# Performance work log

Hardware: AMD Instinct MI355X
Metric: run time of the kernel (lower is better)

## Reference

```python
import jax, jax.numpy as jnp
import numpy as np

N = 8192        # total mesh nodes
M1 = 6000       # nodes set from x (full 3D coords)
M2 = 2000       # nodes set from y (coords 0 and 2 only)
B = 4           # batch
K = 4           # smoothing steps


def setup_inputs() -> dict:
    key = jax.random.key(0)
    k1, k2, k3, k4 = jax.random.split(key, 4)
    # Sparse-ish random symmetric-flavored adjacency, stored dense (as the module does).
    A = (jax.random.uniform(k1, (N, N)) < 0.002).astype(jnp.float32)
    idx = jnp.arange(N)
    # Ring edges guarantee every row has degree >= 1 (avoid divide-by-zero).
    A = A.at[idx, (idx + 1) % N].set(1.0)
    A = A.at[(idx + 1) % N, idx].set(1.0)
    # Diagonal: 1 for first half, 0 for second half -> output mask selects N//2 nodes.
    A = A.at[idx, idx].set((idx < N // 2).astype(jnp.float32))
    # Disjoint index sets for the scatter writes.
    perm = jax.random.permutation(k2, N)
    li1 = perm[:M1].astype(jnp.int64)
    li2 = perm[M1:M1 + M2].astype(jnp.int64)
    x = jax.random.normal(k3, (B, M1 * 3), dtype=jnp.float32)
    y = jax.random.normal(k4, (B, M2 * 2), dtype=jnp.float32)
    temp_zero = jnp.zeros((N, 3), dtype=jnp.float32)
    return {"x": x, "y": y, "edge_matrix": A, "temp_zero": temp_zero,
            "local_indices_1": li1, "local_indices_2": li2, "k": K}


def reference(x, y, edge_matrix, temp_zero, local_indices_1, local_indices_2, k):
    b = x.shape[0]
    # Scatter-build the graph state [B, N, 3].
    temp = jnp.broadcast_to(temp_zero[None], (b,) + temp_zero.shape)
    temp = temp.at[:, local_indices_1, :].set(x.reshape(b, -1, 3))
    y2 = y.reshape(b, -1, 2)
    temp = temp.at[:, local_indices_2, 0].set(y2[:, :, 0])
    temp = temp.at[:, local_indices_2, 2].set(y2[:, :, 1])
    # Degree normalization vector (row sums), computed once.
    deg = jnp.sum(edge_matrix, axis=1)  # [N]
    mesh = temp
    for _ in range(k):
        # smoother: (mesh^T @ A^T)^T == A @ mesh over the node dim, then /degree.
        mesh = jnp.einsum('ij,bjc->bic', edge_matrix, mesh) / deg[None, :, None]
    # Gather rows whose diagonal adjacency entry is zero.
    mask = jnp.diag(edge_matrix) == 0
    return mesh[:, mask, :]
```

## Files before the change

kernel.cpp:

```cpp
#include <hip/hip_runtime.h>

#define NN   8192
#define NNP  (NN + 4)
#define NN3  (NN * 3)
#define NNP3 (NNP * 3)
#define CAP  64
#define M1   6000
#define M2   2000
#define SENT NN

typedef unsigned short u16;

__global__ __launch_bounds__(256) void build_ell(const float* __restrict__ A,
                                                 u16* __restrict__ cols,
                                                 int* __restrict__ nch,
                                                 float* __restrict__ rdeg,
                                                 float* __restrict__ mesh_a,
                                                 float* __restrict__ mesh_b,
                                                 int B) {
    __shared__ int cnt;
    const int row = blockIdx.x;
    const int tid = threadIdx.x;

    {
        const int tot = B * NNP3;
        const int g = blockIdx.x * 256 + tid;
        if (g < tot) mesh_a[g] = 0.f;
        if (blockIdx.x == 0 && tid < B * 12) {
            const int b = tid / 12, r = tid - b * 12;
            mesh_b[b * NNP3 + NN * 3 + r] = 0.f;
        }
    }

    if (tid == 0) cnt = 0;
    __syncthreads();
    const float4* __restrict__ Arow = (const float4*)(A + (size_t)row * NN);
    float4 v[8];
    #pragma unroll
    for (int k = 0; k < 8; ++k) v[k] = Arow[k * 256 + tid];
    u16* __restrict__ crow = cols + row * CAP;
    #pragma unroll
    for (int k = 0; k < 8; ++k) {
        const int base = (k * 256 + tid) * 4;
        if (v[k].x != 0.f) { int p = atomicAdd(&cnt, 1); if (p < CAP) crow[p] = (u16)(base);     }
        if (v[k].y != 0.f) { int p = atomicAdd(&cnt, 1); if (p < CAP) crow[p] = (u16)(base + 1); }
        if (v[k].z != 0.f) { int p = atomicAdd(&cnt, 1); if (p < CAP) crow[p] = (u16)(base + 2); }
        if (v[k].w != 0.f) { int p = atomicAdd(&cnt, 1); if (p < CAP) crow[p] = (u16)(base + 3); }
    }
    __syncthreads();
    int c = cnt;
    if (c > CAP) c = CAP;
    const int padded = (c + 7) & ~7;
    if (tid < padded - c && c + tid < CAP) crow[c + tid] = (u16)SENT;
    if (tid == 0) {
        nch[row]  = padded >> 3;
        rdeg[row] = 1.0f / (float)cnt;
    }
}

__global__ __launch_bounds__(256) void scatter_xy(const float* __restrict__ x,
                                                  const float* __restrict__ y,
                                                  const int* __restrict__ li1,
                                                  const int* __restrict__ li2,
                                                  float* __restrict__ mesh_a, int B) {
    const int g = blockIdx.x * 256 + threadIdx.x;
    const int nx = B * M1 * 3, ny = B * M2 * 2;
    if (g < nx) {
        const int b = g / (M1 * 3);
        const int rem = g - b * (M1 * 3);
        const int j = rem / 3, c = rem - j * 3;
        mesh_a[b * NNP3 + li1[j] * 3 + c] = x[g];
    } else if (g < nx + ny) {
        const int h = g - nx;
        const int b = h / (M2 * 2);
        const int rem = h - b * (M2 * 2);
        const int j = rem / 2, c2 = rem & 1;
        mesh_a[b * NNP3 + li2[j] * 3 + (c2 ? 2 : 0)] = y[h];
    }
}

__global__ __launch_bounds__(256) void spmv_full(const u16* __restrict__ cols,
                                                 const int* __restrict__ nch,
                                                 const float* __restrict__ rdeg,
                                                 const float* __restrict__ src,
                                                 float* __restrict__ dst, int B) {
    const int g = blockIdx.x * 256 + threadIdx.x;
    if (g >= B * NN3) return;
    const int b = g / NN3;
    const int r = g - b * NN3;
    const int i = r / 3, c = r - i * 3;
    const float* __restrict__ mb = src + b * NNP3;
    const uint4* __restrict__ cr = (const uint4*)(cols + i * CAP);
    const int n = nch[i];
    float acc = 0.f;
    for (int ch = 0; ch < n; ++ch) {
        const uint4 q = cr[ch];
        acc += mb[(q.x & 0xFFFF) * 3 + c] + mb[(q.x >> 16) * 3 + c]
             + mb[(q.y & 0xFFFF) * 3 + c] + mb[(q.y >> 16) * 3 + c]
             + mb[(q.z & 0xFFFF) * 3 + c] + mb[(q.z >> 16) * 3 + c]
             + mb[(q.w & 0xFFFF) * 3 + c] + mb[(q.w >> 16) * 3 + c];
    }
    dst[b * NNP3 + i * 3 + c] = acc * rdeg[i];
}

__global__ __launch_bounds__(256) void spmv_last(const u16* __restrict__ cols,
                                                 const int* __restrict__ nch,
                                                 const float* __restrict__ rdeg,
                                                 const float* __restrict__ src,
                                                 float* __restrict__ out, int B) {
    const int H3 = (NN / 2) * 3;
    const int g = blockIdx.x * 256 + threadIdx.x;
    if (g >= B * H3) return;
    const int b = g / H3;
    const int r = g - b * H3;
    const int i2 = r / 3, c = r - i2 * 3;
    const int i = NN / 2 + i2;
    const float* __restrict__ mb = src + b * NNP3;
    const uint4* __restrict__ cr = (const uint4*)(cols + i * CAP);
    const int n = nch[i];
    float acc = 0.f;
    for (int ch = 0; ch < n; ++ch) {
        const uint4 q = cr[ch];
        acc += mb[(q.x & 0xFFFF) * 3 + c] + mb[(q.x >> 16) * 3 + c]
             + mb[(q.y & 0xFFFF) * 3 + c] + mb[(q.y >> 16) * 3 + c]
             + mb[(q.z & 0xFFFF) * 3 + c] + mb[(q.z >> 16) * 3 + c]
             + mb[(q.w & 0xFFFF) * 3 + c] + mb[(q.w >> 16) * 3 + c];
    }
    out[g] = acc * rdeg[i];
}

extern "C" void kernel_launch(void* const* d_in, const int* in_sizes, int n_in,
                              void* d_out, int out_size, void* d_ws, size_t ws_size,
                              hipStream_t stream) {
    const float* x   = (const float*)d_in[0];
    const float* y   = (const float*)d_in[1];
    const float* A   = (const float*)d_in[2];
    const int*   li1 = (const int*)d_in[4];
    const int*   li2 = (const int*)d_in[5];

    const int B = in_sizes[0] / (M1 * 3);

    char* ws = (char*)d_ws;
    u16*   cols   = (u16*)ws;    ws += (size_t)NN * CAP * 2;
    int*   nchv   = (int*)ws;    ws += (size_t)NN * 4;
    float* rdeg   = (float*)ws;  ws += (size_t)NN * 4;
    float* mesh_a = (float*)ws;  ws += (size_t)B * NNP3 * 4;
    float* mesh_b = (float*)ws;

    build_ell<<<NN, 256, 0, stream>>>(A, cols, nchv, rdeg, mesh_a, mesh_b, B);

    const int sc_total = B * M1 * 3 + B * M2 * 2;
    scatter_xy<<<(sc_total + 255) / 256, 256, 0, stream>>>(x, y, li1, li2, mesh_a, B);

    const int full = B * NN3;
    const int nbf = (full + 255) / 256;
    spmv_full<<<nbf, 256, 0, stream>>>(cols, nchv, rdeg, mesh_a, mesh_b, B);
    spmv_full<<<nbf, 256, 0, stream>>>(cols, nchv, rdeg, mesh_b, mesh_a, B);
    spmv_full<<<nbf, 256, 0, stream>>>(cols, nchv, rdeg, mesh_a, mesh_b, B);

    const int half = B * (NN / 2) * 3;
    spmv_last<<<(half + 255) / 256, 256, 0, stream>>>(cols, nchv, rdeg, mesh_b,
                                                      (float*)d_out, B);
}
```

Before: 70.83 us.

## Fuse scatter and four SpMV passes into one cooperative kernel with grid sync

Replaces the dense zero-fill of mesh_a and the scatter kernel with a per-node encoding table (enc) that the first SpMV pass reads to fetch x/y values directly. The four SpMV launches are merged into a single cooperative kernel with grid.sync between steps, which removes launch gaps and the full-buffer memset. In exchange, the first pass adds an extra indirection per neighbour, and the cooperative launch requires all 384 blocks to be co-resident; grid.sync has its own cost.

New measurement: 216.6 us. 206% more time.

```diff
diff --git a/kernel.cpp b/kernel.cpp
--- a/kernel.cpp
+++ b/kernel.cpp
@@ -1,4 +1,7 @@
 #include <hip/hip_runtime.h>
+#include <hip/hip_cooperative_groups.h>
+
+namespace cg = cooperative_groups;
 
 #define NN   8192
 #define NNP  (NN + 4)
@@ -8,6 +11,8 @@
 #define M1   6000
 #define M2   2000
 #define SENT NN
+#define CB   384
+#define CT   256
 
 typedef unsigned short u16;
 
@@ -15,23 +20,29 @@
                                                  u16* __restrict__ cols,
                                                  int* __restrict__ nch,
                                                  float* __restrict__ rdeg,
+                                                 int* __restrict__ enc,
                                                  float* __restrict__ mesh_a,
                                                  float* __restrict__ mesh_b,
+                                                 const int* __restrict__ li1,
+                                                 const int* __restrict__ li2,
                                                  int B) {
-    __shared__ int cnt;
     const int row = blockIdx.x;
     const int tid = threadIdx.x;
 
-    {
-        const int tot = B * NNP3;
-        const int g = blockIdx.x * 256 + tid;
-        if (g < tot) mesh_a[g] = 0.f;
-        if (blockIdx.x == 0 && tid < B * 12) {
+    if (row == NN) {
+        for (int i = tid; i < NNP; i += 256) enc[i] = 0;
+        if (tid < B * 12) {
             const int b = tid / 12, r = tid - b * 12;
+            mesh_a[b * NNP3 + NN * 3 + r] = 0.f;
             mesh_b[b * NNP3 + NN * 3 + r] = 0.f;
         }
+        __syncthreads();
+        for (int j = tid; j < M1; j += 256) enc[li1[j]] = (j << 2) | 1;
+        for (int j = tid; j < M2; j += 256) enc[li2[j]] = (j << 2) | 2;
+        return;
     }
 
+    __shared__ int cnt;
     if (tid == 0) cnt = 0;
     __syncthreads();
     const float4* __restrict__ Arow = (const float4*)(A + (size_t)row * NN);
@@ -58,75 +69,78 @@
     }
 }
 
-__global__ __launch_bounds__(256) void scatter_xy(const float* __restrict__ x,
-                                                  const float* __restrict__ y,
-                                                  const int* __restrict__ li1,
-                                                  const int* __restrict__ li2,
-                                                  float* __restrict__ mesh_a, int B) {
-    const int g = blockIdx.x * 256 + threadIdx.x;
-    const int nx = B * M1 * 3, ny = B * M2 * 2;
-    if (g < nx) {
-        const int b = g / (M1 * 3);
-        const int rem = g - b * (M1 * 3);
-        const int j = rem / 3, c = rem - j * 3;
-        mesh_a[b * NNP3 + li1[j] * 3 + c] = x[g];
-    } else if (g < nx + ny) {
-        const int h = g - nx;
-        const int b = h / (M2 * 2);
-        const int rem = h - b * (M2 * 2);
-        const int j = rem / 2, c2 = rem & 1;
-        mesh_a[b * NNP3 + li2[j] * 3 + (c2 ? 2 : 0)] = y[h];
+#define GATHER8(mb)                                                             \
+    { const uint4 q = cr[ch];                                                   \
+      acc += mb[(q.x & 0xFFFF) * 3 + c] + mb[(q.x >> 16) * 3 + c]               \
+           + mb[(q.y & 0xFFFF) * 3 + c] + mb[(q.y >> 16) * 3 + c]               \
+           + mb[(q.z & 0xFFFF) * 3 + c] + mb[(q.z >> 16) * 3 + c]               \
+           + mb[(q.w & 0xFFFF) * 3 + c] + mb[(q.w >> 16) * 3 + c]; }
+
+__global__ __launch_bounds__(CT) void smooth_coop(
+    const float* __restrict__ x, const float* __restrict__ y,
+    const u16* __restrict__ cols, const int* __restrict__ nch,
+    const float* __restrict__ rdeg, const int* __restrict__ enc,
+    float* __restrict__ mesh_a, float* __restrict__ mesh_b,
+    float* __restrict__ out, int B)
+{
+    cg::grid_group grid = cg::this_grid();
+    const int g = blockIdx.x * CT + threadIdx.x;
+    const bool act = g < B * NN3;
+
+    int b = 0, i = 0, c = 0, n = 0;
+    float rd = 0.f;
+    if (act) {
+        b = g / NN3;
+        const int r = g - b * NN3;
+        i = r / 3; c = r - i * 3;
+        n = nch[i]; rd = rdeg[i];
     }
-}
+    const uint4* __restrict__ cr = (const uint4*)(cols + i * CAP);
 
-__global__ __launch_bounds__(256) void spmv_full(const u16* __restrict__ cols,
-                                                 const int* __restrict__ nch,
-                                                 const float* __restrict__ rdeg,
-                                                 const float* __restrict__ src,
-                                                 float* __restrict__ dst, int B) {
-    const int g = blockIdx.x * 256 + threadIdx.x;
-    if (g >= B * NN3) return;
-    const int b = g / NN3;
-    const int r = g - b * NN3;
-    const int i = r / 3, c = r - i * 3;
-    const float* __restrict__ mb = src + b * NNP3;
-    const uint4* __restrict__ cr = (const uint4*)(cols + i * CAP);
-    const int n = nch[i];
-    float acc = 0.f;
-    for (int ch = 0; ch < n; ++ch) {
-        const uint4 q = cr[ch];
-        acc += mb[(q.x & 0xFFFF) * 3 + c] + mb[(q.x >> 16) * 3 + c]
-             + mb[(q.y & 0xFFFF) * 3 + c] + mb[(q.y >> 16) * 3 + c]
-             + mb[(q.z & 0xFFFF) * 3 + c] + mb[(q.z >> 16) * 3 + c]
-             + mb[(q.w & 0xFFFF) * 3 + c] + mb[(q.w >> 16) * 3 + c];
+    if (act) {
+        const int bM1 = b * M1, bM2 = b * M2;
+        float acc = 0.f;
+        for (int ch = 0; ch < n; ++ch) {
+            const uint4 q = cr[ch];
+            const int jj[8] = { (int)(q.x & 0xFFFF), (int)(q.x >> 16),
+                                (int)(q.y & 0xFFFF), (int)(q.y >> 16),
+                                (int)(q.z & 0xFFFF), (int)(q.z >> 16),
+                                (int)(q.w & 0xFFFF), (int)(q.w >> 16) };
+            #pragma unroll
+            for (int t = 0; t < 8; ++t) {
+                const int e = enc[jj[t]];
+                float v = 0.f;
+                if (e & 1)                       v = x[(bM1 + (e >> 2)) * 3 + c];
+                else if ((e & 2) && (c != 1))    v = y[(bM2 + (e >> 2)) * 2 + (c >> 1)];
+                acc += v;
+            }
+        }
+        mesh_a[b * NNP3 + i * 3 + c] = acc * rd;
     }
-    dst[b * NNP3 + i * 3 + c] = acc * rdeg[i];
-}
+    grid.sync();
 
-__global__ __launch_bounds__(256) void spmv_last(const u16* __restrict__ cols,
-                                                 const int* __restrict__ nch,
-                                                 const float* __restrict__ rdeg,
-                                                 const float* __restrict__ src,
-                                                 float* __restrict__ out, int B) {
-    const int H3 = (NN / 2) * 3;
-    const int g = blockIdx.x * 256 + threadIdx.x;
-    if (g >= B * H3) return;
-    const int b = g / H3;
-    const int r = g - b * H3;
-    const int i2 = r / 3, c = r - i2 * 3;
-    const int i = NN / 2 + i2;
-    const float* __restrict__ mb = src + b * NNP3;
-    const uint4* __restrict__ cr = (const uint4*)(cols + i * CAP);
-    const int n = nch[i];
-    float acc = 0.f;
-    for (int ch = 0; ch < n; ++ch) {
-        const uint4 q = cr[ch];
-        acc += mb[(q.x & 0xFFFF) * 3 + c] + mb[(q.x >> 16) * 3 + c]
-             + mb[(q.y & 0xFFFF) * 3 + c] + mb[(q.y >> 16) * 3 + c]
-             + mb[(q.z & 0xFFFF) * 3 + c] + mb[(q.z >> 16) * 3 + c]
-             + mb[(q.w & 0xFFFF) * 3 + c] + mb[(q.w >> 16) * 3 + c];
+    if (act) {
+        const float* __restrict__ mb = mesh_a + b * NNP3;
+        float acc = 0.f;
+        for (int ch = 0; ch < n; ++ch) GATHER8(mb);
+        mesh_b[b * NNP3 + i * 3 + c] = acc * rd;
     }
-    out[g] = acc * rdeg[i];
+    grid.sync();
+
+    if (act) {
+        const float* __restrict__ mb = mesh_b + b * NNP3;
+        float acc = 0.f;
+        for (int ch = 0; ch < n; ++ch) GATHER8(mb);
+        mesh_a[b * NNP3 + i * 3 + c] = acc * rd;
+    }
+    grid.sync();
+
+    if (act && i >= NN / 2) {
+        const float* __restrict__ mb = mesh_a + b * NNP3;
+        float acc = 0.f;
+        for (int ch = 0; ch < n; ++ch) GATHER8(mb);
+        out[((size_t)b * (NN / 2) + (i - NN / 2)) * 3 + c] = acc * rd;
+    }
 }
 
 extern "C" void kernel_launch(void* const* d_in, const int* in_sizes, int n_in,
@@ -138,27 +152,22 @@
     const int*   li1 = (const int*)d_in[4];
     const int*   li2 = (const int*)d_in[5];
 
-    const int B = in_sizes[0] / (M1 * 3);
+    int B = in_sizes[0] / (M1 * 3);
 
     char* ws = (char*)d_ws;
     u16*   cols   = (u16*)ws;    ws += (size_t)NN * CAP * 2;
     int*   nchv   = (int*)ws;    ws += (size_t)NN * 4;
     float* rdeg   = (float*)ws;  ws += (size_t)NN * 4;
+    int*   enc    = (int*)ws;    ws += (size_t)(NNP + 4) * 4;
     float* mesh_a = (float*)ws;  ws += (size_t)B * NNP3 * 4;
     float* mesh_b = (float*)ws;
+    float* outp   = (float*)d_out;
 
-    build_ell<<<NN, 256, 0, stream>>>(A, cols, nchv, rdeg, mesh_a, mesh_b, B);
+    build_ell<<<NN + 1, 256, 0, stream>>>(A, cols, nchv, rdeg, enc,
+                                          mesh_a, mesh_b, li1, li2, B);
 
-    const int sc_total = B * M1 * 3 + B * M2 * 2;
-    scatter_xy<<<(sc_total + 255) / 256, 256, 0, stream>>>(x, y, li1, li2, mesh_a, B);
-
-    const int full = B * NN3;
-    const int nbf = (full + 255) / 256;
-    spmv_full<<<nbf, 256, 0, stream>>>(cols, nchv, rdeg, mesh_a, mesh_b, B);
-    spmv_full<<<nbf, 256, 0, stream>>>(cols, nchv, rdeg, mesh_b, mesh_a, B);
-    spmv_full<<<nbf, 256, 0, stream>>>(cols, nchv, rdeg, mesh_a, mesh_b, B);
-
-    const int half = B * (NN / 2) * 3;
-    spmv_last<<<(half + 255) / 256, 256, 0, stream>>>(cols, nchv, rdeg, mesh_b,
-                                                      (float*)d_out, B);
+    void* args[] = { &x, &y, &cols, &nchv, &rdeg, &enc,
+                     &mesh_a, &mesh_b, &outp, &B };
+    hipLaunchCooperativeKernel((void*)smooth_coop, dim3(CB), dim3(CT),
+                               args, 0, stream);
 }
```
